# Kernel tuning notes

Hardware: AMD Instinct MI355X
Metric: run time of the kernel (lower is better)

## Reference

```python
import jax, jax.numpy as jnp
import numpy as np

KNN_K = 16
EPS = 1e-5


def _knn_idx(p, k):
    # p: [B,3,N] -> idx [B,N,k] of nearest neighbors (self excluded)
    pt = jnp.swapaxes(p, 1, 2)                      # [B,N,3]
    xx = jnp.sum(pt * pt, axis=-1)                  # [B,N]
    inner = jnp.einsum('bnd,bmd->bnm', pt, pt)      # [B,N,N]
    dist = -(xx[:, :, None] - 2.0 * inner + xx[:, None, :])  # -||pi-pj||^2
    N = pt.shape[1]
    dist = dist - 1e9 * jnp.eye(N, dtype=dist.dtype)
    return jax.lax.top_k(dist, k)[1]


def _ln(x, g, b):
    mu = jnp.mean(x, axis=-1, keepdims=True)
    var = jnp.mean((x - mu) ** 2, axis=-1, keepdims=True)
    return (x - mu) * jax.lax.rsqrt(var + EPS) * g + b


_gather = jax.vmap(lambda a, i: a[i])  # a:[N,C], i:[N,k] -> [N,k,C]


def setup_inputs() -> dict:
    key = jax.random.key(0)
    ks = jax.random.split(key, 24)
    Cin, C, B, N = 64, 128, 8, 2048
    s = lambda k_, shp, fan: jax.random.normal(k_, shp, jnp.float32) * (1.0 / np.sqrt(fan))
    return {
        'x': jax.random.normal(ks[0], (B, Cin, N), jnp.float32),
        'p': jax.random.normal(ks[1], (B, 3, N), jnp.float32),
        'Win': s(ks[2], (C, Cin), Cin), 'bin_': jnp.zeros((C,), jnp.float32),
        'Wq': s(ks[3], (C, C), C), 'Wk': s(ks[4], (C, C), C), 'Wv': s(ks[5], (C, C), C),
        'Wd1': s(ks[6], (C, 3), 3), 'bd1': jnp.zeros((C,), jnp.float32),
        'Wd2': s(ks[7], (C, C), C), 'bd2': jnp.zeros((C,), jnp.float32),
        'Wa': s(ks[8], (C, C), C), 'ba': jnp.zeros((C,), jnp.float32),
        'g1': jnp.ones((C,), jnp.float32), 'b1': jnp.zeros((C,), jnp.float32),
        'g2': jnp.ones((C,), jnp.float32), 'b2': jnp.zeros((C,), jnp.float32),
        'Wf1': s(ks[9], (4 * C, C), C), 'bf1': jnp.zeros((4 * C,), jnp.float32),
        'Wf2': s(ks[10], (C, 4 * C), 4 * C), 'bf2': jnp.zeros((C,), jnp.float32),
    }


def reference(x, p, Win, bin_, Wq, Wk, Wv, Wd1, bd1, Wd2, bd2, Wa, ba,
              g1, b1, g2, b2, Wf1, bf1, Wf2, bf2) -> jnp.ndarray:
    B, _, N = x.shape
    k = min(KNN_K, max(1, N - 1))
    # in_proj (conv1x1 == per-point linear); work in [B,N,C]
    h = jnp.einsum('oc,bcn->bno', Win, x) + bin_          # [B,N,C]
    hn = _ln(h, g1, b1)
    idx = _knn_idx(p, k)                                  # [B,N,k] (int)
    q = hn @ Wq.T                                         # [B,N,C]
    k_all = hn @ Wk.T
    v_all = hn @ Wv.T
    k_j = _gather(k_all, idx)                             # [B,N,k,C]
    v_j = _gather(v_all, idx)
    pt = jnp.swapaxes(p, 1, 2)                            # [B,N,3]
    p_j = _gather(pt, idx)                                # [B,N,k,3]
    rel = pt[:, :, None, :] - p_j                         # [B,N,k,3]
    d = jax.nn.relu(rel @ Wd1.T + bd1) @ Wd2.T + bd2      # [B,N,k,C]
    logits = (q[:, :, None, :] - k_j + d) @ Wa.T + ba     # [B,N,k,C]
    a = jax.nn.softmax(logits, axis=2)                    # softmax over neighbors
    y = jnp.sum(a * (v_j + d), axis=2)                    # [B,N,C]
    h = h + y
    h2 = _ln(h, g2, b2)
    h = h + jax.nn.relu(h2 @ Wf1.T + bf1) @ Wf2.T + bf2
    return jnp.swapaxes(h, 1, 2)                          # [B,C,N]
```

## Files before the change

kernel.cpp:

```cpp
#include <hip/hip_runtime.h>

typedef __bf16 bf16_t;
typedef __bf16 bf16x8 __attribute__((ext_vector_type(8)));
typedef __bf16 bf16x4 __attribute__((ext_vector_type(4)));
typedef __bf16 bf16x2 __attribute__((ext_vector_type(2)));
typedef float  f32x4  __attribute__((ext_vector_type(4)));

#define MFMA16(a,b,c) __builtin_amdgcn_mfma_f32_16x16x32_bf16((a),(b),(c),0,0,0)

#define BB 8
#define NN 2048
#define CC 128
#define CIN 64
#define KNB 16
#define BNT (BB*NN)

static __device__ __forceinline__ int remap256(int x) { return ((x & 7) << 5) | (x >> 3); }

static __device__ __forceinline__ bf16x8 cvt8(const float* src) {
  f32x4 a0 = *(const f32x4*)src;
  f32x4 a1 = *(const f32x4*)(src + 4);
  bf16x8 fr;
  fr[0] = (__bf16)a0[0]; fr[1] = (__bf16)a0[1]; fr[2] = (__bf16)a0[2]; fr[3] = (__bf16)a0[3];
  fr[4] = (__bf16)a1[0]; fr[5] = (__bf16)a1[1]; fr[6] = (__bf16)a1[2]; fr[7] = (__bf16)a1[3];
  return fr;
}

__global__ __launch_bounds__(256) void inproj_compw_k(
    const float* __restrict__ x, const float* __restrict__ Win, const float* __restrict__ bin,
    const float* __restrict__ g1, const float* __restrict__ b1,
    bf16_t* __restrict__ hb, bf16_t* __restrict__ hnb,
    const float* __restrict__ Wq, const float* __restrict__ Wk, const float* __restrict__ Wv,
    const float* __restrict__ Wd2, const float* __restrict__ Wa,
    const float* __restrict__ Wf1, const float* __restrict__ Wf2, const float* __restrict__ bd2,
    bf16_t* __restrict__ Wqab, bf16_t* __restrict__ Wkab, bf16_t* __restrict__ Wvb,
    bf16_t* __restrict__ Wd2b, bf16_t* __restrict__ Wd2ab,
    bf16_t* __restrict__ Wf1b, bf16_t* __restrict__ Wf2b, float* __restrict__ bd2a) {
  __shared__ bf16_t As[64 * 72];
  __shared__ bf16_t Bs[128 * 72];
  __shared__ float hs[64 * 132];
  int t = threadIdx.x;
  if (blockIdx.x >= 256) {
    int bi = blockIdx.x - 256;
    if (bi < 32) {
      int mat = bi >> 3, xi = bi & 7;
      int nel = (mat >= 2) ? 65536 : 16384;
      const float* S = mat == 0 ? Wv : mat == 1 ? Wd2 : mat == 2 ? Wf1 : Wf2;
      bf16_t* D = mat == 0 ? Wvb : mat == 1 ? Wd2b : mat == 2 ? Wf1b : Wf2b;
      for (int i = xi * 256 + t; i * 8 < nel; i += 2048)
        *(bf16x8*)(D + i * 8) = cvt8(S + i * 8);
    } else if (bi < 80) {
      int pi = bi - 32, mat = pi >> 4, xi = pi & 15;
      const float* R = mat == 0 ? Wq : mat == 1 ? Wk : Wd2;
      bf16_t* D = mat == 0 ? Wqab : mat == 1 ? Wkab : Wd2ab;
      int c = xi * 8 + (t >> 5);
      int i0 = (t & 31) * 4;
      const float* war = Wa + (size_t)c * CC;
      f32x4 acc = {0.f, 0.f, 0.f, 0.f};
      #pragma unroll 4
      for (int e = 0; e < CC; ++e) {
        float a = war[e];
        f32x4 bq = *(const f32x4*)(R + (size_t)e * CC + i0);
        acc[0] = fmaf(a, bq[0], acc[0]);
        acc[1] = fmaf(a, bq[1], acc[1]);
        acc[2] = fmaf(a, bq[2], acc[2]);
        acc[3] = fmaf(a, bq[3], acc[3]);
      }
      bf16x4 o;
      o[0] = (__bf16)acc[0]; o[1] = (__bf16)acc[1];
      o[2] = (__bf16)acc[2]; o[3] = (__bf16)acc[3];
      *(bf16x4*)(D + (size_t)c * CC + i0) = o;
    } else {
      if (t < 128) {
        float s = 0.f;
        const float* war = Wa + (size_t)t * CC;
        #pragma unroll 4
        for (int e = 0; e < CC; ++e) s = fmaf(war[e], bd2[e], s);
        bd2a[t] = s;
      }
    }
    return;
  }
  int lane = t & 63, w = t >> 6, quad = lane >> 4, l15 = lane & 15;
  int mBase = remap256(blockIdx.x) * 64;
  int b = mBase >> 11, n0 = mBase & (NN - 1);
  const float* xb = x + (size_t)b * CIN * NN;
  {
    int k = t >> 2, part = t & 3;
    #pragma unroll
    for (int i = 0; i < 4; ++i) {
      f32x4 v = *(const f32x4*)(xb + (size_t)k * NN + n0 + part * 16 + i * 4);
      #pragma unroll
      for (int j2 = 0; j2 < 4; ++j2) As[(part * 16 + i * 4 + j2) * 72 + k] = (__bf16)v[j2];
    }
  }
  {
    int row = t >> 1, seg = (t & 1) * 32;
    #pragma unroll
    for (int i = 0; i < 4; ++i)
      *(bf16x8*)(&Bs[row * 72 + seg + i * 8]) = cvt8(Win + (size_t)row * CIN + seg + i * 8);
  }
  __syncthreads();
  f32x4 acc[2][4] = {};
  #pragma unroll
  for (int s = 0; s < 2; ++s) {
    bf16x8 af[4];
    #pragma unroll
    for (int mt = 0; mt < 4; ++mt)
      af[mt] = *(const bf16x8*)(&As[(mt * 16 + l15) * 72 + s * 32 + quad * 8]);
    #pragma unroll
    for (int t2 = 0; t2 < 2; ++t2) {
      bf16x8 bfr = *(const bf16x8*)(&Bs[((w * 2 + t2) * 16 + l15) * 72 + s * 32 + quad * 8]);
      #pragma unroll
      for (int mt = 0; mt < 4; ++mt) acc[t2][mt] = MFMA16(af[mt], bfr, acc[t2][mt]);
    }
  }
  #pragma unroll
  for (int t2 = 0; t2 < 2; ++t2) {
    int col = (w * 2 + t2) * 16 + l15;
    float bv = bin[col];
    #pragma unroll
    for (int mt = 0; mt < 4; ++mt)
      #pragma unroll
      for (int reg = 0; reg < 4; ++reg)
        hs[(mt * 16 + quad * 4 + reg) * 132 + col] = acc[t2][mt][reg] + bv;
  }
  __syncthreads();
  {
    int row = t >> 2, c0 = (t & 3) * 32;
    float v[32];
    #pragma unroll
    for (int i = 0; i < 8; ++i) *(f32x4*)(v + i * 4) = *(const f32x4*)(&hs[row * 132 + c0 + i * 4]);
    float s1 = 0.f, s2 = 0.f;
    #pragma unroll
    for (int i = 0; i < 32; ++i) { s1 += v[i]; s2 += v[i] * v[i]; }
    s1 += __shfl_xor(s1, 1); s1 += __shfl_xor(s1, 2);
    s2 += __shfl_xor(s2, 1); s2 += __shfl_xor(s2, 2);
    float mu = s1 * (1.f / CC);
    float var = s2 * (1.f / CC) - mu * mu;
    float rs = rsqrtf(var + 1e-5f);
    bf16_t* hrow = hb + (size_t)(mBase + row) * CC + c0;
    #pragma unroll
    for (int i = 0; i < 4; ++i) {
      bf16x8 ho;
      #pragma unroll
      for (int j = 0; j < 8; ++j) ho[j] = (__bf16)v[i * 8 + j];
      *(bf16x8*)(hrow + i * 8) = ho;
    }
    bf16_t* hnrow = hnb + (size_t)(mBase + row) * CC + c0;
    #pragma unroll
    for (int i = 0; i < 4; ++i) {
      f32x4 g4a = ((const f32x4*)g1)[(c0 >> 2) + i * 2],     g4b = ((const f32x4*)g1)[(c0 >> 2) + i * 2 + 1];
      f32x4 b4a = ((const f32x4*)b1)[(c0 >> 2) + i * 2],     b4b = ((const f32x4*)b1)[(c0 >> 2) + i * 2 + 1];
      bf16x8 o;
      #pragma unroll
      for (int j = 0; j < 4; ++j) o[j]     = (__bf16)((v[i * 8 + j]     - mu) * rs * g4a[j] + b4a[j]);
      #pragma unroll
      for (int j = 0; j < 4; ++j) o[4 + j] = (__bf16)((v[i * 8 + 4 + j] - mu) * rs * g4b[j] + b4b[j]);
      *(bf16x8*)(hnrow + i * 8) = o;
    }
  }
}

static __device__ __forceinline__ void cas(double& a, double& b) {
  double lo = fmin(a, b), hi = fmax(a, b); a = lo; b = hi;
}
#define S8(K,o) \
  cas(K[o+0],K[o+1]); cas(K[o+2],K[o+3]); cas(K[o+4],K[o+5]); cas(K[o+6],K[o+7]); \
  cas(K[o+0],K[o+2]); cas(K[o+1],K[o+3]); cas(K[o+4],K[o+6]); cas(K[o+5],K[o+7]); \
  cas(K[o+1],K[o+2]); cas(K[o+5],K[o+6]); \
  cas(K[o+0],K[o+4]); cas(K[o+1],K[o+5]); cas(K[o+2],K[o+6]); cas(K[o+3],K[o+7]); \
  cas(K[o+2],K[o+4]); cas(K[o+3],K[o+5]); \
  cas(K[o+1],K[o+2]); cas(K[o+3],K[o+4]); cas(K[o+5],K[o+6]);
#define M8(K,a,b) \
  K[a+0]=fmin(K[a+0],K[b+7]); K[a+1]=fmin(K[a+1],K[b+6]); K[a+2]=fmin(K[a+2],K[b+5]); K[a+3]=fmin(K[a+3],K[b+4]); \
  K[a+4]=fmin(K[a+4],K[b+3]); K[a+5]=fmin(K[a+5],K[b+2]); K[a+6]=fmin(K[a+6],K[b+1]); K[a+7]=fmin(K[a+7],K[b+0]); \
  cas(K[a+0],K[a+4]); cas(K[a+1],K[a+5]); cas(K[a+2],K[a+6]); cas(K[a+3],K[a+7]); \
  cas(K[a+0],K[a+2]); cas(K[a+1],K[a+3]); cas(K[a+4],K[a+6]); cas(K[a+5],K[a+7]); \
  cas(K[a+0],K[a+1]); cas(K[a+2],K[a+3]); cas(K[a+4],K[a+5]); cas(K[a+6],K[a+7]);

static __device__ void knn_impl(float* sp, const float* __restrict__ p,
                                int* __restrict__ idxo, int bid) {
  float* px = sp; float* py = sp + NN; float* pz = sp + 2 * NN;
  int t = threadIdx.x;
  int b = bid >> 9;
  int g = bid & 511;
  const float* pb = p + (size_t)b * 3 * NN;
  for (int i = t; i < NN; i += 256) { px[i] = pb[i]; py[i] = pb[NN + i]; pz[i] = pb[2 * NN + i]; }
  __syncthreads();
  int w = t >> 6, lane = t & 63;
  int n = g * 4 + w;
  float pnx = px[n], pny = py[n], pnz = pz[n];
  double key[32];
  #pragma unroll
  for (int s = 0; s < 32; ++s) {
    int m = s * 64 + lane;
    float dx = pnx - px[m], dy = pny - py[m], dz = pnz - pz[m];
    float dist = dx * dx + dy * dy + dz * dz;
    unsigned db = (m == n) ? 0x7F800000u : __float_as_uint(dist);
    key[s] = __hiloint2double((int)db, m);
  }
  S8(key, 0); S8(key, 8); S8(key, 16); S8(key, 24);
  M8(key, 0, 8); M8(key, 16, 24); M8(key, 0, 16);
  const double DINF = __hiloint2double(0x7F900000, 0);
  int* myout = idxo + ((size_t)b * NN + n) * KNB;
  #pragma unroll 1
  for (int r = 0; r < 16; ++r) {
    double gm = key[0];
    #pragma unroll
    for (int off = 1; off < 64; off <<= 1) {
      double o = __shfl_xor(gm, off);
      gm = fmin(gm, o);
    }
    if (lane == 0) myout[r] = __double2loint(gm);
    bool win = (key[0] == gm);
    key[0] = win ? key[1] : key[0];
    key[1] = win ? key[2] : key[1];
    key[2] = win ? key[3] : key[2];
    key[3] = win ? key[4] : key[3];
    key[4] = win ? key[5] : key[4];
    key[5] = win ? key[6] : key[5];
    key[6] = win ? key[7] : key[6];
    key[7] = win ? DINF   : key[7];
  }
}

template<int EPI>
static __device__ void gemm_body(bf16_t* As, bf16_t* Bs,
    const bf16_t* __restrict__ Ab, const bf16_t* __restrict__ Wb, const float* __restrict__ bias,
    float* __restrict__ outF, bf16_t* __restrict__ outB, const bf16_t* __restrict__ resid,
    int mBase, int nBase, int Ncol, int Kdim) {
  int t = threadIdx.x;
  int lane = t & 63, w = t >> 6, quad = lane >> 4, l15 = lane & 15;
  int r = t >> 2, seg = (t & 3) * 8;
  f32x4 acc[4] = {{0,0,0,0},{0,0,0,0},{0,0,0,0},{0,0,0,0}};
  for (int k0 = 0; k0 < Kdim; k0 += 32) {
    __syncthreads();
    *(bf16x8*)(&As[r * 40 + seg]) = *(const bf16x8*)(Ab + (size_t)(mBase + r) * Kdim + k0 + seg);
    *(bf16x8*)(&Bs[r * 40 + seg]) = *(const bf16x8*)(Wb + (size_t)(nBase + r) * Kdim + k0 + seg);
    __syncthreads();
    bf16x8 bfr = *(const bf16x8*)(&Bs[(w * 16 + l15) * 40 + quad * 8]);
    #pragma unroll
    for (int mt = 0; mt < 4; ++mt) {
      bf16x8 afr = *(const bf16x8*)(&As[(mt * 16 + l15) * 40 + quad * 8]);
      acc[mt] = MFMA16(afr, bfr, acc[mt]);
    }
  }
  int n = nBase + w * 16 + l15;
  float bv = bias ? bias[n] : 0.f;
  #pragma unroll
  for (int mt = 0; mt < 4; ++mt) {
    #pragma unroll
    for (int reg = 0; reg < 4; ++reg) {
      int m = mBase + mt * 16 + quad * 4 + reg;
      float val = acc[mt][reg] + bv;
      if (EPI == 1) {
        outB[(size_t)m * Ncol + n] = (__bf16)fmaxf(val, 0.f);
      } else if (EPI == 3) {
        outB[(size_t)m * Ncol + n] = (__bf16)val;
      } else {
        val += (float)resid[(size_t)m * CC + n];
        int bo = m >> 11, np = m & (NN - 1);
        outF[((size_t)bo * CC + n) * NN + np] = val;
      }
    }
  }
}

template<int EPI>
__global__ __launch_bounds__(256) void gemm_k(
    const bf16_t* __restrict__ Ab, const bf16_t* __restrict__ Wb, const float* __restrict__ bias,
    float* __restrict__ outF, bf16_t* __restrict__ outB, const bf16_t* __restrict__ resid,
    int Ncol, int Kdim) {
  __shared__ bf16_t As[64 * 40];
  __shared__ bf16_t Bs[64 * 40];
  gemm_body<EPI>(As, Bs, Ab, Wb, bias, outF, outB, resid,
                 remap256(blockIdx.x) * 64, blockIdx.y * 64, Ncol, Kdim);
}

__global__ __launch_bounds__(256) void knn_qkv_k(
    const float* __restrict__ p, int* __restrict__ idxo,
    const bf16_t* __restrict__ hnb,
    const bf16_t* __restrict__ Wqab, const bf16_t* __restrict__ Wkab, const bf16_t* __restrict__ Wvb,
    bf16_t* __restrict__ qb, bf16_t* __restrict__ kb, bf16_t* __restrict__ vb) {
  __shared__ __align__(16) char smem[3 * NN * 4];
  if (blockIdx.x < 4096) {
    knn_impl((float*)smem, p, idxo, blockIdx.x);
  } else {
    bf16_t* As = (bf16_t*)smem;
    bf16_t* Bs = As + 64 * 40;
    int bx = blockIdx.x - 4096;
    int yy = bx >> 8, xx = bx & 255;
    int sel = yy >> 1;
    int mB = remap256(xx) * 64, nB = (yy & 1) * 64;
    if (sel == 0)      gemm_body<3>(As, Bs, hnb, Wqab, nullptr, nullptr, qb, nullptr, mB, nB, CC, CC);
    else if (sel == 1) gemm_body<3>(As, Bs, hnb, Wkab, nullptr, nullptr, kb, nullptr, mB, nB, CC, CC);
    else               gemm_body<3>(As, Bs, hnb, Wvb, nullptr, nullptr, vb, nullptr, mB, nB, CC, CC);
  }
}

__global__ __launch_bounds__(256, 3) void attn_k(
    const bf16_t* __restrict__ qbuf, const bf16_t* __restrict__ kbuf, const bf16_t* __restrict__ vbuf,
    const float* __restrict__ p, const int* __restrict__ idx,
    const float* __restrict__ Wd1, const float* __restrict__ bd1,
    const bf16_t* __restrict__ Wd2b, const float* __restrict__ bd2,
    const bf16_t* __restrict__ Wd2ab, const float* __restrict__ bd2a,
    const float* __restrict__ ba,
    const float* __restrict__ g2, const float* __restrict__ b2,
    const bf16_t* __restrict__ hb, bf16_t* __restrict__ hresb, bf16_t* __restrict__ h2) {
  __shared__ bf16_t ts[64 * 136];
  __shared__ float hrs[4 * 128];
  __shared__ f32x4 wd1s[128];
  __shared__ f32x4 rels4[64];
  __shared__ int idxs[64];
  int t = threadIdx.x;
  int lane = t & 63, w = t >> 6, quad = lane >> 4, l15 = lane & 15;
  int batch = blockIdx.x & 7, grp = blockIdx.x >> 3;
  int bn0 = batch * NN + grp * 4;
  const float* pb = p + (size_t)batch * 3 * NN;
  int col0 = w * 32 + l15;
  int col1 = col0 + 16;

  if (t < 64) {
    int jj = idx[(size_t)bn0 * KNB + t];
    idxs[t] = jj;
    int npt = grp * 4 + (t >> 4);
    f32x4 rv;
    rv[0] = pb[npt]          - pb[jj];
    rv[1] = pb[NN + npt]     - pb[NN + jj];
    rv[2] = pb[2 * NN + npt] - pb[2 * NN + jj];
    rv[3] = 0.f;
    rels4[t] = rv;
  }
  if (t < 128) {
    f32x4 wv;
    wv[0] = Wd1[t * 3]; wv[1] = Wd1[t * 3 + 1]; wv[2] = Wd1[t * 3 + 2]; wv[3] = bd1[t];
    wd1s[t] = wv;
  }
  __syncthreads();

  {
    int row = t >> 2, cseg = (t & 3) * 32;
    f32x4 rv = rels4[row];
    #pragma unroll
    for (int i = 0; i < 4; ++i) {
      bf16x8 u8;
      #pragma unroll
      for (int j = 0; j < 8; ++j) {
        f32x4 wv = wd1s[cseg + i * 8 + j];
        float tv = fmaf(wv[0], rv[0], fmaf(wv[1], rv[1], fmaf(wv[2], rv[2], wv[3])));
        u8[j] = (__bf16)fmaxf(tv, 0.f);
      }
      *(bf16x8*)(&ts[row * 136 + cseg + i * 8]) = u8;
    }
  }
  __syncthreads();

  f32x4 acca[2][4] = {};
  {
    bf16x8 Bf[2][4];
    #pragma unroll
    for (int t2 = 0; t2 < 2; ++t2) {
      int row = w * 32 + t2 * 16 + l15;
      #pragma unroll
      for (int s = 0; s < 4; ++s)
        Bf[t2][s] = *(const bf16x8*)(Wd2ab + (size_t)row * CC + s * 32 + quad * 8);
    }
    #pragma unroll
    for (int s = 0; s < 4; ++s) {
      bf16x8 af[4];
      #pragma unroll
      for (int mt = 0; mt < 4; ++mt)
        af[mt] = *(const bf16x8*)(&ts[(mt * 16 + l15) * 136 + s * 32 + quad * 8]);
      #pragma unroll
      for (int t2 = 0; t2 < 2; ++t2)
        #pragma unroll
        for (int mt = 0; mt < 4; ++mt)
          acca[t2][mt] = MFMA16(af[mt], Bf[t2][s], acca[t2][mt]);
    }
  }

  {
    float qv[2][4];
    #pragma unroll
    for (int mt = 0; mt < 4; ++mt) {
      qv[0][mt] = (float)qbuf[(size_t)(bn0 + mt) * CC + col0];
      qv[1][mt] = (float)qbuf[(size_t)(bn0 + mt) * CC + col1];
    }
    float kreg[2][4][4];
    #pragma unroll
    for (int mt = 0; mt < 4; ++mt)
      #pragma unroll
      for (int reg = 0; reg < 4; ++reg) {
        size_t base = (size_t)(batch * NN + idxs[mt * 16 + quad * 4 + reg]) * CC;
        kreg[0][mt][reg] = (float)kbuf[base + col0];
        kreg[1][mt][reg] = (float)kbuf[base + col1];
      }
    #pragma unroll
    for (int t2 = 0; t2 < 2; ++t2) {
      int col = t2 ? col1 : col0;
      float cA = bd2a[col] + ba[col];
      #pragma unroll
      for (int mt = 0; mt < 4; ++mt)
        #pragma unroll
        for (int reg = 0; reg < 4; ++reg)
          acca[t2][mt][reg] += qv[t2][mt] - kreg[t2][mt][reg] + cA;
    }
  }

  f32x4 accd[2][4] = {};
  {
    bf16x8 Bf[2][4];
    #pragma unroll
    for (int t2 = 0; t2 < 2; ++t2) {
      int row = w * 32 + t2 * 16 + l15;
      #pragma unroll
      for (int s = 0; s < 4; ++s)
        Bf[t2][s] = *(const bf16x8*)(Wd2b + (size_t)row * CC + s * 32 + quad * 8);
    }
    #pragma unroll
    for (int s = 0; s < 4; ++s) {
      bf16x8 af[4];
      #pragma unroll
      for (int mt = 0; mt < 4; ++mt)
        af[mt] = *(const bf16x8*)(&ts[(mt * 16 + l15) * 136 + s * 32 + quad * 8]);
      #pragma unroll
      for (int t2 = 0; t2 < 2; ++t2)
        #pragma unroll
        for (int mt = 0; mt < 4; ++mt)
          accd[t2][mt] = MFMA16(af[mt], Bf[t2][s], accd[t2][mt]);
    }
  }

  float vreg[2][4][4];
  #pragma unroll
  for (int mt = 0; mt < 4; ++mt)
    #pragma unroll
    for (int reg = 0; reg < 4; ++reg) {
      size_t base = (size_t)(batch * NN + idxs[mt * 16 + quad * 4 + reg]) * CC;
      vreg[0][mt][reg] = (float)vbuf[base + col0];
      vreg[1][mt][reg] = (float)vbuf[base + col1];
    }
  float hv[2][4];
  if (quad == 0) {
    #pragma unroll
    for (int mt = 0; mt < 4; ++mt) {
      hv[0][mt] = (float)hb[(size_t)(bn0 + mt) * CC + col0];
      hv[1][mt] = (float)hb[(size_t)(bn0 + mt) * CC + col1];
    }
  }

  #pragma unroll
  for (int t2 = 0; t2 < 2; ++t2) {
    int col = t2 ? col1 : col0;
    float bv = bd2[col];
    #pragma unroll
    for (int mt = 0; mt < 4; ++mt) {
      float lv0 = acca[t2][mt][0], lv1 = acca[t2][mt][1];
      float lv2 = acca[t2][mt][2], lv3 = acca[t2][mt][3];
      float mx = fmaxf(fmaxf(lv0, lv1), fmaxf(lv2, lv3));
      mx = fmaxf(mx, __shfl_xor(mx, 16));
      mx = fmaxf(mx, __shfl_xor(mx, 32));
      float e0 = __expf(lv0 - mx), e1 = __expf(lv1 - mx);
      float e2 = __expf(lv2 - mx), e3 = __expf(lv3 - mx);
      float ss = e0 + e1 + e2 + e3;
      ss += __shfl_xor(ss, 16); ss += __shfl_xor(ss, 32);
      float yv = e0 * (vreg[t2][mt][0] + accd[t2][mt][0])
               + e1 * (vreg[t2][mt][1] + accd[t2][mt][1])
               + e2 * (vreg[t2][mt][2] + accd[t2][mt][2])
               + e3 * (vreg[t2][mt][3] + accd[t2][mt][3]);
      yv += __shfl_xor(yv, 16); yv += __shfl_xor(yv, 32);
      if (quad == 0) {
        float hvv = hv[t2][mt] + yv / ss + bv;
        hresb[(size_t)(bn0 + mt) * CC + col] = (__bf16)hvv;
        hrs[mt * 128 + col] = hvv;
      }
    }
  }
  __syncthreads();

  {
    int c0 = lane * 2;
    float v0 = hrs[w * 128 + c0], v1 = hrs[w * 128 + c0 + 1];
    float s1 = v0 + v1, s2 = v0 * v0 + v1 * v1;
    #pragma unroll
    for (int off = 1; off < 64; off <<= 1) { s1 += __shfl_xor(s1, off); s2 += __shfl_xor(s2, off); }
    float mu = s1 * (1.f / CC);
    float var = s2 * (1.f / CC) - mu * mu;
    float rs = rsqrtf(var + 1e-5f);
    bf16x2 o;
    o[0] = (__bf16)((v0 - mu) * rs * g2[c0] + b2[c0]);
    o[1] = (__bf16)((v1 - mu) * rs * g2[c0 + 1] + b2[c0 + 1]);
    *(bf16x2*)(h2 + (size_t)(bn0 + w) * CC + c0) = o;
  }
}

extern "C" void kernel_launch(void* const* d_in, const int* in_sizes, int n_in,
                              void* d_out, int out_size, void* d_ws, size_t ws_size,
                              hipStream_t stream) {
  const float* x   = (const float*)d_in[0];
  const float* p   = (const float*)d_in[1];
  const float* Win = (const float*)d_in[2];
  const float* bin = (const float*)d_in[3];
  const float* Wq  = (const float*)d_in[4];
  const float* Wk  = (const float*)d_in[5];
  const float* Wv  = (const float*)d_in[6];
  const float* Wd1 = (const float*)d_in[7];
  const float* bd1 = (const float*)d_in[8];
  const float* Wd2 = (const float*)d_in[9];
  const float* bd2 = (const float*)d_in[10];
  const float* Wa  = (const float*)d_in[11];
  const float* ba  = (const float*)d_in[12];
  const float* g1  = (const float*)d_in[13];
  const float* b1  = (const float*)d_in[14];
  const float* g2  = (const float*)d_in[15];
  const float* b2  = (const float*)d_in[16];
  const float* Wf1 = (const float*)d_in[17];
  const float* bf1 = (const float*)d_in[18];
  const float* Wf2 = (const float*)d_in[19];
  const float* bf2 = (const float*)d_in[20];
  float* out = (float*)d_out;

  const size_t SZ = (size_t)BNT * CC;
  float* wsf = (float*)d_ws;
  bf16_t* hb    = (bf16_t*)wsf;
  bf16_t* hnb   = (bf16_t*)(wsf + SZ / 2);
  bf16_t* hresb = hnb;
  bf16_t* qb    = (bf16_t*)(wsf + SZ);
  bf16_t* kb    = (bf16_t*)(wsf + SZ + SZ / 2);
  bf16_t* vb    = (bf16_t*)(wsf + 2 * SZ);
  bf16_t* g     = (bf16_t*)(wsf + SZ);
  bf16_t* h2    = (bf16_t*)(wsf + 3 * SZ);
  int*    idxw  = (int*)(wsf + 3 * SZ + SZ / 2);
  bf16_t* Wqab  = (bf16_t*)(idxw + (size_t)BNT * KNB);
  bf16_t* Wkab  = Wqab  + 16384;
  bf16_t* Wvb   = Wkab  + 16384;
  bf16_t* Wd2b  = Wvb   + 16384;
  bf16_t* Wd2ab = Wd2b  + 16384;
  bf16_t* Wf1b  = Wd2ab + 16384;
  bf16_t* Wf2b  = Wf1b  + 65536;
  float*  bd2a  = (float*)(Wf2b + 65536);

  inproj_compw_k<<<256 + 81, 256, 0, stream>>>(x, Win, bin, g1, b1, hb, hnb,
                                               Wq, Wk, Wv, Wd2, Wa, Wf1, Wf2, bd2,
                                               Wqab, Wkab, Wvb, Wd2b, Wd2ab, Wf1b, Wf2b, bd2a);
  knn_qkv_k<<<4096 + 1536, 256, 0, stream>>>(p, idxw, hnb, Wqab, Wkab, Wvb, qb, kb, vb);
  attn_k<<<BNT / 4, 256, 0, stream>>>(qb, kb, vb, p, idxw, Wd1, bd1, Wd2b, bd2, Wd2ab, bd2a,
                                      ba, g2, b2, hb, hresb, h2);
  gemm_k<1><<<dim3(BNT / 64, 8), 256, 0, stream>>>(h2, Wf1b, bf1, nullptr, g, nullptr, 4 * CC, CC);
  gemm_k<2><<<dim3(BNT / 64, 2), 256, 0, stream>>>(g, Wf2b, bf2, out, nullptr, hresb, CC, 4 * CC);
}
```

Measured before the change: 260.7 us.

## Stage gathered K/V neighbor rows through LDS with vectorized row loads

Replaces the per-lane scalar bf16 gathers of neighbor K and V rows with coalesced 16-byte row loads that are staged through a new shared-memory tile, then read back in MFMA fragment layout. The K load is issued before the relu(Wd1) computation and the V load before the first MFMA to overlap global latency with compute. It adds about 17 KB of LDS and two extra barriers, which may reduce occupancy under the 3-blocks-per-CU launch bound.

Measured after the change: 299.9 us. 15.0% more time.

```diff
diff --git a/kernel.cpp b/kernel.cpp
--- a/kernel.cpp
+++ b/kernel.cpp
@@ -309,6 +309,7 @@
     const float* __restrict__ g2, const float* __restrict__ b2,
     const bf16_t* __restrict__ hb, bf16_t* __restrict__ hresb, bf16_t* __restrict__ h2) {
   __shared__ bf16_t ts[64 * 136];
+  __shared__ bf16_t ks[64 * 136];
   __shared__ float hrs[4 * 128];
   __shared__ f32x4 wd1s[128];
   __shared__ f32x4 rels4[64];
@@ -339,22 +340,63 @@
   }
   __syncthreads();
 
-  {
-    int row = t >> 2, cseg = (t & 3) * 32;
-    f32x4 rv = rels4[row];
+  int srow = t >> 2, sseg = (t & 3) * 32;
+  size_t srowbase = (size_t)(batch * NN + idxs[srow]) * CC + sseg;
+
+  bf16x8 kst0, kst1, kst2, kst3;
+  {
+    const bf16_t* krow = kbuf + srowbase;
+    kst0 = *(const bf16x8*)(krow);
+    kst1 = *(const bf16x8*)(krow + 8);
+    kst2 = *(const bf16x8*)(krow + 16);
+    kst3 = *(const bf16x8*)(krow + 24);
+  }
+
+  {
+    f32x4 rv = rels4[srow];
     #pragma unroll
     for (int i = 0; i < 4; ++i) {
       bf16x8 u8;
       #pragma unroll
       for (int j = 0; j < 8; ++j) {
-        f32x4 wv = wd1s[cseg + i * 8 + j];
+        f32x4 wv = wd1s[sseg + i * 8 + j];
         float tv = fmaf(wv[0], rv[0], fmaf(wv[1], rv[1], fmaf(wv[2], rv[2], wv[3])));
         u8[j] = (__bf16)fmaxf(tv, 0.f);
       }
-      *(bf16x8*)(&ts[row * 136 + cseg + i * 8]) = u8;
-    }
-  }
-  __syncthreads();
+      *(bf16x8*)(&ts[srow * 136 + sseg + i * 8]) = u8;
+    }
+  }
+  *(bf16x8*)(&ks[srow * 136 + sseg])      = kst0;
+  *(bf16x8*)(&ks[srow * 136 + sseg + 8])  = kst1;
+  *(bf16x8*)(&ks[srow * 136 + sseg + 16]) = kst2;
+  *(bf16x8*)(&ks[srow * 136 + sseg + 24]) = kst3;
+  __syncthreads();
+
+  float kreg[2][4][4];
+  #pragma unroll
+  for (int mt = 0; mt < 4; ++mt)
+    #pragma unroll
+    for (int reg = 0; reg < 4; ++reg) {
+      int rr = mt * 16 + quad * 4 + reg;
+      kreg[0][mt][reg] = (float)ks[rr * 136 + col0];
+      kreg[1][mt][reg] = (float)ks[rr * 136 + col1];
+    }
+
+  bf16x8 vst0, vst1, vst2, vst3;
+  {
+    const bf16_t* vrow = vbuf + srowbase;
+    vst0 = *(const bf16x8*)(vrow);
+    vst1 = *(const bf16x8*)(vrow + 8);
+    vst2 = *(const bf16x8*)(vrow + 16);
+    vst3 = *(const bf16x8*)(vrow + 24);
+  }
+
+  float qv[2][4];
+  #pragma unroll
+  for (int mt = 0; mt < 4; ++mt) {
+    qv[0][mt] = (float)qbuf[(size_t)(bn0 + mt) * CC + col0];
+    qv[1][mt] = (float)qbuf[(size_t)(bn0 + mt) * CC + col1];
+  }
 
   f32x4 acca[2][4] = {};
   {
@@ -380,31 +422,39 @@
     }
   }
 
-  {
-    float qv[2][4];
+  #pragma unroll
+  for (int t2 = 0; t2 < 2; ++t2) {
+    int col = t2 ? col1 : col0;
+    float cA = bd2a[col] + ba[col];
+    #pragma unroll
+    for (int mt = 0; mt < 4; ++mt)
+      #pragma unroll
+      for (int reg = 0; reg < 4; ++reg)
+        acca[t2][mt][reg] += qv[t2][mt] - kreg[t2][mt][reg] + cA;
+  }
+
+  __syncthreads();
+  *(bf16x8*)(&ks[srow * 136 + sseg])      = vst0;
+  *(bf16x8*)(&ks[srow * 136 + sseg + 8])  = vst1;
+  *(bf16x8*)(&ks[srow * 136 + sseg + 16]) = vst2;
+  *(bf16x8*)(&ks[srow * 136 + sseg + 24]) = vst3;
+  __syncthreads();
+
+  float vreg[2][4][4];
+  #pragma unroll
+  for (int mt = 0; mt < 4; ++mt)
+    #pragma unroll
+    for (int reg = 0; reg < 4; ++reg) {
+      int rr = mt * 16 + quad * 4 + reg;
+      vreg[0][mt][reg] = (float)ks[rr * 136 + col0];
+      vreg[1][mt][reg] = (float)ks[rr * 136 + col1];
+    }
+  float hv[2][4];
+  if (quad == 0) {
     #pragma unroll
     for (int mt = 0; mt < 4; ++mt) {
-      qv[0][mt] = (float)qbuf[(size_t)(bn0 + mt) * CC + col0];
-      qv[1][mt] = (float)qbuf[(size_t)(bn0 + mt) * CC + col1];
-    }
-    float kreg[2][4][4];
-    #pragma unroll
-    for (int mt = 0; mt < 4; ++mt)
-      #pragma unroll
-      for (int reg = 0; reg < 4; ++reg) {
-        size_t base = (size_t)(batch * NN + idxs[mt * 16 + quad * 4 + reg]) * CC;
-        kreg[0][mt][reg] = (float)kbuf[base + col0];
-        kreg[1][mt][reg] = (float)kbuf[base + col1];
-      }
-    #pragma unroll
-    for (int t2 = 0; t2 < 2; ++t2) {
-      int col = t2 ? col1 : col0;
-      float cA = bd2a[col] + ba[col];
-      #pragma unroll
-      for (int mt = 0; mt < 4; ++mt)
-        #pragma unroll
-        for (int reg = 0; reg < 4; ++reg)
-          acca[t2][mt][reg] += qv[t2][mt] - kreg[t2][mt][reg] + cA;
+      hv[0][mt] = (float)hb[(size_t)(bn0 + mt) * CC + col0];
+      hv[1][mt] = (float)hb[(size_t)(bn0 + mt) * CC + col1];
     }
   }
 
@@ -429,24 +479,6 @@
         #pragma unroll
         for (int mt = 0; mt < 4; ++mt)
           accd[t2][mt] = MFMA16(af[mt], Bf[t2][s], accd[t2][mt]);
-    }
-  }
-
-  float vreg[2][4][4];
-  #pragma unroll
-  for (int mt = 0; mt < 4; ++mt)
-    #pragma unroll
-    for (int reg = 0; reg < 4; ++reg) {
-      size_t base = (size_t)(batch * NN + idxs[mt * 16 + quad * 4 + reg]) * CC;
-      vreg[0][mt][reg] = (float)vbuf[base + col0];
-      vreg[1][mt][reg] = (float)vbuf[base + col1];
-    }
-  float hv[2][4];
-  if (quad == 0) {
-    #pragma unroll
-    for (int mt = 0; mt < 4; ++mt) {
-      hv[0][mt] = (float)hb[(size_t)(bn0 + mt) * CC + col0];
-      hv[1][mt] = (float)hb[(size_t)(bn0 + mt) * CC + col1];
     }
   }
 
```
